# Optimization experiments

Hardware: AMD Instinct MI355X
Metric: run time of the kernel (lower is better)

The kernel has to match this reference:

```python
import jax, jax.numpy as jnp
import numpy as np

N_NODES = 100000
N_EDGES = 6400000


def setup_inputs() -> dict:
    key = jax.random.key(0)
    k1, k2, k3, k4, k5, k6 = jax.random.split(key, 6)
    x = jax.random.normal(k1, (N_NODES, 20), dtype=jnp.float32)
    edge_index = jax.random.randint(k2, (2, N_EDGES), 0, N_NODES, dtype=jnp.int64)
    # Glorot-style init for GCNConv weights, zero bias (PyG default)
    W1 = jax.random.normal(k3, (20, 16), dtype=jnp.float32) * (1.0 / np.sqrt(20))
    b1 = jnp.zeros((16,), dtype=jnp.float32)
    W2 = jax.random.normal(k4, (16, 2), dtype=jnp.float32) * (1.0 / np.sqrt(16))
    b2 = jnp.zeros((2,), dtype=jnp.float32)
    return {"x": x, "edge_index": edge_index, "W1": W1, "b1": b1, "W2": W2, "b2": b2}


def gcn_conv(x, row, col, W, b, num_nodes):
    # x' = D^{-1/2} (A + I) D^{-1/2} X W + b  (PyG GCNConv with self-loops)
    xw = x @ W  # [N, out]
    ones = jnp.ones_like(row, dtype=xw.dtype)
    deg = jax.ops.segment_sum(ones, row, num_segments=num_nodes)  # [N]
    dinv = jnp.where(deg > 0, jax.lax.rsqrt(deg), 0.0)
    norm = dinv[row] * dinv[col]  # [E+N]
    msg = xw[col] * norm[:, None]  # gather + scale
    out = jax.ops.segment_sum(msg, row, num_segments=num_nodes)  # scatter-add
    return out + b


def reference(x, edge_index, W1, b1, W2, b2):
    num_nodes = x.shape[0]
    self_loops = jnp.arange(num_nodes, dtype=edge_index.dtype)
    row = jnp.concatenate([edge_index[0], self_loops])  # target nodes
    col = jnp.concatenate([edge_index[1], self_loops])  # source nodes
    h = gcn_conv(x, row, col, W1, b1, num_nodes)
    h = jax.nn.relu(h)
    # F.dropout(x, training=self.training): identity in eval mode
    h = gcn_conv(h, row, col, W2, b2, num_nodes)
    return jax.nn.log_softmax(h, axis=1)
```

## Files before the change

### kernel.cpp

```cpp
#include <hip/hip_runtime.h>
#include <math.h>


#define XF 20
#define F1 16
#define F2 2
#define RPB 128
#define KMAX 800
#define KP   784
#define TILE 8192
#define EPT 16
#define NJMAX 800
#define CAP 9216
#define BPAD 16

__device__ __forceinline__ unsigned bf16rne(float f) {
    unsigned u = __float_as_uint(f);
    return (u + 0x7FFFu + ((u >> 16) & 1u)) >> 16;
}
__device__ __forceinline__ float bflo(unsigned w) { return __uint_as_float(w << 16); }
__device__ __forceinline__ float bfhi(unsigned w) { return __uint_as_float(w & 0xFFFF0000u); }

__global__ __launch_bounds__(512) void passA_kernel(const int* __restrict__ rows,
                                                    const int* __restrict__ cols,
                                                    int* __restrict__ bhist,
                                                    int* __restrict__ lbt,
                                                    unsigned int* __restrict__ csrtmp,
                                                    int E, int K) {
    __shared__ unsigned int stage[TILE];
    __shared__ int hist[KMAX];
    __shared__ int tsum[512];
    int t = threadIdx.x;
    int bj = blockIdx.x;
    for (int k = t; k < K; k += 512) hist[k] = 0;
    __syncthreads();
    int e0 = bj * TILE;
    int e1 = min(e0 + TILE, E);
    int n = e1 - e0;
    int rloc[EPT];
    #pragma unroll
    for (int it = 0; it < EPT; it++) {
        int e = e0 + it * 512 + t;
        if (e < e1) {
            int r = rows[e];
            rloc[it] = r;
            atomicAdd(&hist[r >> 7], 1);
        }
    }
    __syncthreads();
    int k0 = 2 * t, k1 = 2 * t + 1;
    int v0 = (k0 < K) ? hist[k0] : 0;
    int v1 = (k1 < K) ? hist[k1] : 0;
    int s = v0 + v1;
    tsum[t] = s;
    __syncthreads();
    for (int d = 1; d < 512; d <<= 1) {
        int u = (t >= d) ? tsum[t - d] : 0;
        __syncthreads();
        tsum[t] += u;
        __syncthreads();
    }
    int run = tsum[t] - s;
    long long lrow = (long long)bj * KP;
    if (k0 < K) {
        hist[k0] = run;  lbt[lrow + k0] = run;
        if (v0) atomicAdd(&bhist[k0 * BPAD], v0);
    }
    if (k1 < K) {
        hist[k1] = run + v0;  lbt[lrow + k1] = run + v0;
        if (v1) atomicAdd(&bhist[k1 * BPAD], v1);
    }
    if (t == 0) lbt[lrow + K] = n;
    __syncthreads();
    #pragma unroll
    for (int it = 0; it < EPT; it++) {
        int e = e0 + it * 512 + t;
        if (e < e1) {
            int r = rloc[it];
            int c = cols[e];
            int pos = atomicAdd(&hist[r >> 7], 1);
            stage[pos] = ((unsigned int)c << 7) | (unsigned int)(r & 127);
        }
    }
    __syncthreads();
    for (int ss = t; ss < n; ss += 512)
        csrtmp[(size_t)e0 + ss] = stage[ss];
}

__global__ void bscan_kernel(const int* __restrict__ bhist, int K, int E,
                             int* __restrict__ bbase) {
    __shared__ int tsum[256];
    int t = threadIdx.x;
    int vals[4];
    int s = 0;
    #pragma unroll
    for (int j = 0; j < 4; j++) {
        int idx = t * 4 + j;
        vals[j] = (idx < K) ? bhist[idx * BPAD] : 0;
        s += vals[j];
    }
    tsum[t] = s;
    __syncthreads();
    for (int d = 1; d < 256; d <<= 1) {
        int u = (t >= d) ? tsum[t - d] : 0;
        __syncthreads();
        tsum[t] += u;
        __syncthreads();
    }
    int run = tsum[t] - s;
    #pragma unroll
    for (int j = 0; j < 4; j++) {
        int idx = t * 4 + j;
        if (idx < K) bbase[idx] = run;
        run += vals[j];
    }
    if (t == 0) bbase[K] = E;
}

__global__ __launch_bounds__(512) void passB_kernel(const int* __restrict__ lbt,
                                                    const unsigned int* __restrict__ csrtmp,
                                                    const int* __restrict__ bbase,
                                                    unsigned int* __restrict__ csr,
                                                    int* __restrict__ rowptr,
                                                    float* __restrict__ dinv,
                                                    int N, int K, int E, int nj) {
    __shared__ unsigned int stage[CAP];
    __shared__ int segoff[NJMAX];
    __shared__ int stagepos[NJMAX + 1];
    __shared__ int dcnt[RPB];
    __shared__ int rp[RPB];
    __shared__ int cur[RPB];
    __shared__ int tsum[512];
    int b = blockIdx.x, t = threadIdx.x;
    int lo = b << 7;
    if (t < RPB) { dcnt[t] = 0; cur[t] = 0; }
    int a0 = 2 * t, a1 = 2 * t + 1;
    int la = 0, lb2 = 0;
    if (a0 < nj) {
        const int* lp = lbt + (long long)a0 * KP + b;
        int o0 = lp[0], o1 = lp[1];
        segoff[a0] = o0; la = o1 - o0;
    }
    if (a1 < nj) {
        const int* lp = lbt + (long long)a1 * KP + b;
        int o0 = lp[0], o1 = lp[1];
        segoff[a1] = o0; lb2 = o1 - o0;
    }
    int s = la + lb2;
    tsum[t] = s;
    __syncthreads();
    for (int d = 1; d < 512; d <<= 1) {
        int u = (t >= d) ? tsum[t - d] : 0;
        __syncthreads();
        tsum[t] += u;
        __syncthreads();
    }
    int run = tsum[t] - s;
    if (a0 < nj) stagepos[a0] = run;
    if (a1 < nj) stagepos[a1] = run + la;
    if (t == 511) stagepos[nj] = tsum[511];
    __syncthreads();
    int cnt = min(stagepos[nj], CAP);
    int sw = t >> 3, ln = t & 7;
    for (int seg = sw; seg < nj; seg += 64) {
        int sp = stagepos[seg];
        int len = stagepos[seg + 1] - sp;
        if (sp + len > CAP) len = max(0, CAP - sp);
        size_t src = (size_t)seg * TILE + segoff[seg];
        for (int e2 = ln; e2 < len; e2 += 8) {
            unsigned int p = csrtmp[src + e2];
            stage[sp + e2] = p;
            atomicAdd(&dcnt[p & 127u], 1);
        }
    }
    __syncthreads();
    int gb = bbase[b];
    if (t < 64) {
        int v0 = dcnt[2 * t], v1 = dcnt[2 * t + 1];
        int ss = v0 + v1;
        int sc = ss;
        #pragma unroll
        for (int d = 1; d < 64; d <<= 1) {
            int u = __shfl_up(sc, d);
            if (t >= d) sc += u;
        }
        int excl = gb + sc - ss;
        rp[2 * t] = excl;
        rp[2 * t + 1] = excl + v0;
        int i0 = lo + 2 * t, i1 = i0 + 1;
        if (i0 < N) { rowptr[i0] = excl;      dinv[i0] = rsqrtf((float)v0 + 1.0f); }
        if (i1 < N) { rowptr[i1] = excl + v0; dinv[i1] = rsqrtf((float)v1 + 1.0f); }
        if (t == 0 && b == K - 1) rowptr[N] = E;
    }
    __syncthreads();
    for (int ss = t; ss < cnt; ss += 512) {
        unsigned int p = stage[ss];
        int rr = (int)(p & 127u);
        int dst = rp[rr] + atomicAdd(&cur[rr], 1);
        csr[dst] = p >> 7;
    }
}

__global__ void xw1_kernel(const float* __restrict__ x, const float* __restrict__ W1,
                           const float* __restrict__ dinv, unsigned int* __restrict__ y1h,
                           int N) {
    __shared__ float Ws[XF * F1];
    for (int k = threadIdx.x; k < XF * F1; k += blockDim.x) Ws[k] = W1[k];
    __syncthreads();
    int i = blockIdx.x * blockDim.x + threadIdx.x;
    if (i >= N) return;
    const float4* xv = (const float4*)(x + (size_t)i * XF);
    float xr[XF];
    #pragma unroll
    for (int q = 0; q < 5; q++) {
        float4 v = xv[q];
        xr[q*4+0] = v.x; xr[q*4+1] = v.y; xr[q*4+2] = v.z; xr[q*4+3] = v.w;
    }
    float d = dinv[i];
    float out[F1];
    #pragma unroll
    for (int j = 0; j < F1; j++) {
        float a = 0.f;
        #pragma unroll
        for (int k = 0; k < XF; k++) a += xr[k] * Ws[k * F1 + j];
        out[j] = a * d;
    }
    unsigned int w[8];
    #pragma unroll
    for (int q = 0; q < 8; q++)
        w[q] = bf16rne(out[2*q]) | (bf16rne(out[2*q+1]) << 16);
    uint4* o = (uint4*)(y1h + (size_t)i * 8);
    o[0] = make_uint4(w[0], w[1], w[2], w[3]);
    o[1] = make_uint4(w[4], w[5], w[6], w[7]);
}

__global__ __launch_bounds__(256) void gather16_kernel(const int* __restrict__ rowptr,
                                                       const unsigned int* __restrict__ csr,
                                                       const unsigned int* __restrict__ y1h,
                                                       const float* __restrict__ dinv,
                                                       const float* __restrict__ b1,
                                                       const float* __restrict__ W2,
                                                       float* __restrict__ y2, int N) {
    __shared__ float W2s[F1 * F2];
    if (threadIdx.x < F1 * F2) W2s[threadIdx.x] = W2[threadIdx.x];
    __syncthreads();
    int sub = threadIdx.x >> 5;
    int l = threadIdx.x & 31;
    int i = blockIdx.x * 8 + sub;
    if (i >= N) return;
    int half = l & 1, es = l >> 1;
    int start = rowptr[i], end = rowptr[i + 1];
    const uint4* Y = (const uint4*)y1h;
    float acc[8] = {0.f, 0.f, 0.f, 0.f, 0.f, 0.f, 0.f, 0.f};
    for (int slot = start + es; slot < end; slot += 16) {
        int c = (int)csr[slot];
        uint4 w = Y[(size_t)c * 2 + half];
        acc[0] += bflo(w.x); acc[1] += bfhi(w.x);
        acc[2] += bflo(w.y); acc[3] += bfhi(w.y);
        acc[4] += bflo(w.z); acc[5] += bfhi(w.z);
        acc[6] += bflo(w.w); acc[7] += bfhi(w.w);
    }
    #pragma unroll
    for (int m = 2; m <= 16; m <<= 1) {
        #pragma unroll
        for (int k = 0; k < 8; k++) acc[k] += __shfl_xor(acc[k], m);
    }
    if (l < 2) {
        float d = dinv[i];
        uint4 w = Y[(size_t)i * 2 + l];
        float self[8] = { bflo(w.x), bfhi(w.x), bflo(w.y), bfhi(w.y),
                          bflo(w.z), bfhi(w.z), bflo(w.w), bfhi(w.w) };
        float4 bl = ((const float4*)b1)[l * 2];
        float4 bh = ((const float4*)b1)[l * 2 + 1];
        float bb[8] = { bl.x, bl.y, bl.z, bl.w, bh.x, bh.y, bh.z, bh.w };
        float p0 = 0.f, p1 = 0.f;
        #pragma unroll
        for (int k = 0; k < 8; k++) {
            float hv = fmaxf(d * (acc[k] + self[k]) + bb[k], 0.f);
            p0 += hv * W2s[(l * 8 + k) * 2];
            p1 += hv * W2s[(l * 8 + k) * 2 + 1];
        }
        float q0 = __shfl_xor(p0, 1);
        float q1 = __shfl_xor(p1, 1);
        if (l == 0)
            ((float2*)y2)[i] = make_float2((p0 + q0) * d, (p1 + q1) * d);
    }
}

__global__ __launch_bounds__(256) void gather2_kernel(const int* __restrict__ rowptr,
                                                      const unsigned int* __restrict__ csr,
                                                      const float* __restrict__ y2,
                                                      const float* __restrict__ dinv,
                                                      const float* __restrict__ b2,
                                                      float* __restrict__ out, int N) {
    int sub = threadIdx.x >> 5;
    int l = threadIdx.x & 31;
    int i = blockIdx.x * 8 + sub;
    if (i >= N) return;
    int start = rowptr[i], end = rowptr[i + 1];
    float a0 = 0.f, a1 = 0.f;
    for (int slot = start + l; slot < end; slot += 32) {
        int c = (int)csr[slot];
        float2 v = ((const float2*)y2)[c];
        a0 += v.x;
        a1 += v.y;
    }
    #pragma unroll
    for (int m = 16; m > 0; m >>= 1) {
        a0 += __shfl_xor(a0, m);
        a1 += __shfl_xor(a1, m);
    }
    if (l == 0) {
        float d = dinv[i];
        float2 yi = ((const float2*)y2)[i];
        float v0 = d * (a0 + yi.x) + b2[0];
        float v1 = d * (a1 + yi.y) + b2[1];
        float mm = fmaxf(v0, v1);
        float lse = mm + logf(expf(v0 - mm) + expf(v1 - mm));
        ((float2*)out)[i] = make_float2(v0 - lse, v1 - lse);
    }
}

static inline size_t align256(size_t x) { return (x + 255) & ~(size_t)255; }

extern "C" void kernel_launch(void* const* d_in, const int* in_sizes, int n_in,
                              void* d_out, int out_size, void* d_ws, size_t ws_size,
                              hipStream_t stream) {
    const float* x  = (const float*)d_in[0];
    const int*   ei = (const int*)d_in[1];
    const float* W1 = (const float*)d_in[2];
    const float* b1 = (const float*)d_in[3];
    const float* W2 = (const float*)d_in[4];
    const float* b2 = (const float*)d_in[5];
    float* out = (float*)d_out;

    const int N = in_sizes[0] / XF;
    const int E = in_sizes[1] / 2;
    const int* rows = ei;
    const int* cols = ei + E;
    const int K = (N + RPB - 1) >> 7;
    const int nj = (E + TILE - 1) / TILE;

    char* ws = (char*)d_ws;
    size_t off = 0;
    int*   bhist   = (int*)(ws + off);   off = align256(off + (size_t)KMAX * BPAD * 4);
    size_t zero_bytes = off;
    int*   bbase   = (int*)(ws + off);   off = align256(off + (size_t)(KMAX + 1) * 4);
    int*   rowptr  = (int*)(ws + off);   off = align256(off + (size_t)(N + 1) * 4);
    float* dinv    = (float*)(ws + off); off = align256(off + (size_t)N * 4);
    int*   lbt     = (int*)(ws + off);   off = align256(off + (size_t)nj * KP * 4);
    unsigned int* csr = (unsigned int*)(ws + off); off = align256(off + (size_t)E * 4);
    size_t tmp0 = off;
    unsigned int* csrtmp = (unsigned int*)(ws + tmp0);
    unsigned int* y1h = (unsigned int*)(ws + tmp0);
    float* y2 = (float*)(ws + align256(tmp0 + (size_t)N * 8 * 4));

    hipMemsetAsync(d_ws, 0, zero_bytes, stream);

    const int B = 256;
    const int nbN = (N + B - 1) / B;
    const int nbW = (N + 7) / 8;

    passA_kernel<<<nj, 512, 0, stream>>>(rows, cols, bhist, lbt, csrtmp, E, K);
    bscan_kernel<<<1, B, 0, stream>>>(bhist, K, E, bbase);
    passB_kernel<<<K, 512, 0, stream>>>(lbt, csrtmp, bbase, csr, rowptr, dinv, N, K, E, nj);
    xw1_kernel<<<nbN, B, 0, stream>>>(x, W1, dinv, y1h, N);
    gather16_kernel<<<nbW, B, 0, stream>>>(rowptr, csr, y1h, dinv, b1, W2, y2, N);
    gather2_kernel<<<nbW, B, 0, stream>>>(rowptr, csr, y2, dinv, b2, out, N);
}
```

Before: 278.0 us.

## Transpose bucket offset table and privatize passB histogram across four sub-groups

Adds a tiled transpose kernel so passB can read each block's per-tile segment offsets contiguously with int2 loads, replacing strided column reads. passB now copies edges into shared memory first, then counts them in four padded per-thread-group histograms to cut LDS atomic contention. The scatter uses per-group cursors derived from the combined prefix sums. In exchange it adds an extra kernel launch, extra workspace, and an extra pass over the shared-memory stage.

New measurement: 283.9 us. +2.1%, slower.

```diff
diff --git a/kernel.cpp b/kernel.cpp
--- a/kernel.cpp
+++ b/kernel.cpp
@@ -8,6 +8,7 @@
 #define RPB 128
 #define KMAX 800
 #define KP   784
+#define NJP  800
 #define TILE 8192
 #define EPT 16
 #define NJMAX 800
@@ -117,7 +118,31 @@
     if (t == 0) bbase[K] = E;
 }
 
-__global__ __launch_bounds__(512) void passB_kernel(const int* __restrict__ lbt,
+__global__ __launch_bounds__(256) void transpose_kernel(const int* __restrict__ lbt,
+                                                        int* __restrict__ lbtT,
+                                                        int nj, int K) {
+    __shared__ int tile[64][65];
+    int tx = threadIdx.x & 63, ty = threadIdx.x >> 6;
+    int bk = blockIdx.x * 64;
+    int bb = blockIdx.y * 64;
+    #pragma unroll
+    for (int r = 0; r < 16; r++) {
+        int row = bb + ty * 16 + r;
+        int col = bk + tx;
+        if (row < nj && col <= K)
+            tile[ty * 16 + r][tx] = lbt[(long long)row * KP + col];
+    }
+    __syncthreads();
+    #pragma unroll
+    for (int r = 0; r < 16; r++) {
+        int orow = bk + ty * 16 + r;
+        int ocol = bb + tx;
+        if (orow <= K && ocol < nj)
+            lbtT[(long long)orow * NJP + ocol] = tile[tx][ty * 16 + r];
+    }
+}
+
+__global__ __launch_bounds__(512) void passB_kernel(const int* __restrict__ lbtT,
                                                     const unsigned int* __restrict__ csrtmp,
                                                     const int* __restrict__ bbase,
                                                     unsigned int* __restrict__ csr,
@@ -127,24 +152,24 @@
     __shared__ unsigned int stage[CAP];
     __shared__ int segoff[NJMAX];
     __shared__ int stagepos[NJMAX + 1];
-    __shared__ int dcnt[RPB];
-    __shared__ int rp[RPB];
-    __shared__ int cur[RPB];
+    __shared__ int dcnt4[4 * 132];
+    __shared__ int cur4[4 * 132];
+    __shared__ int rp4[4 * 128];
     __shared__ int tsum[512];
     int b = blockIdx.x, t = threadIdx.x;
     int lo = b << 7;
-    if (t < RPB) { dcnt[t] = 0; cur[t] = 0; }
-    int a0 = 2 * t, a1 = 2 * t + 1;
+    for (int k = t; k < 4 * 132; k += 512) { dcnt4[k] = 0; cur4[k] = 0; }
+    int a0 = 2 * t, a1 = a0 + 1;
     int la = 0, lb2 = 0;
-    if (a0 < nj) {
-        const int* lp = lbt + (long long)a0 * KP + b;
-        int o0 = lp[0], o1 = lp[1];
-        segoff[a0] = o0; la = o1 - o0;
-    }
     if (a1 < nj) {
-        const int* lp = lbt + (long long)a1 * KP + b;
-        int o0 = lp[0], o1 = lp[1];
-        segoff[a1] = o0; lb2 = o1 - o0;
+        int2 s2 = ((const int2*)(lbtT + (long long)b * NJP))[t];
+        int2 e2 = ((const int2*)(lbtT + (long long)(b + 1) * NJP))[t];
+        segoff[a0] = s2.x; segoff[a1] = s2.y;
+        la = e2.x - s2.x;  lb2 = e2.y - s2.y;
+    } else if (a0 < nj) {
+        int o0 = lbtT[(long long)b * NJP + a0];
+        segoff[a0] = o0;
+        la = lbtT[(long long)(b + 1) * NJP + a0] - o0;
     }
     int s = la + lb2;
     tsum[t] = s;
@@ -167,36 +192,44 @@
         int len = stagepos[seg + 1] - sp;
         if (sp + len > CAP) len = max(0, CAP - sp);
         size_t src = (size_t)seg * TILE + segoff[seg];
-        for (int e2 = ln; e2 < len; e2 += 8) {
-            unsigned int p = csrtmp[src + e2];
-            stage[sp + e2] = p;
-            atomicAdd(&dcnt[p & 127u], 1);
-        }
-    }
+        for (int e2 = ln; e2 < len; e2 += 8)
+            stage[sp + e2] = csrtmp[src + e2];
+    }
+    __syncthreads();
+    int g = t >> 7;
+    for (int ss = t; ss < cnt; ss += 512)
+        atomicAdd(&dcnt4[g * 132 + (int)(stage[ss] & 127u)], 1);
     __syncthreads();
     int gb = bbase[b];
     if (t < 64) {
-        int v0 = dcnt[2 * t], v1 = dcnt[2 * t + 1];
-        int ss = v0 + v1;
-        int sc = ss;
+        int r0 = 2 * t, r1 = r0 + 1;
+        int c00 = dcnt4[r0], c10 = dcnt4[132 + r0], c20 = dcnt4[264 + r0], c30 = dcnt4[396 + r0];
+        int c01 = dcnt4[r1], c11 = dcnt4[132 + r1], c21 = dcnt4[264 + r1], c31 = dcnt4[396 + r1];
+        int v0 = c00 + c10 + c20 + c30;
+        int v1 = c01 + c11 + c21 + c31;
+        int ssum = v0 + v1;
+        int sc = ssum;
         #pragma unroll
         for (int d = 1; d < 64; d <<= 1) {
             int u = __shfl_up(sc, d);
             if (t >= d) sc += u;
         }
-        int excl = gb + sc - ss;
-        rp[2 * t] = excl;
-        rp[2 * t + 1] = excl + v0;
-        int i0 = lo + 2 * t, i1 = i0 + 1;
-        if (i0 < N) { rowptr[i0] = excl;      dinv[i0] = rsqrtf((float)v0 + 1.0f); }
-        if (i1 < N) { rowptr[i1] = excl + v0; dinv[i1] = rsqrtf((float)v1 + 1.0f); }
+        int excl = gb + sc - ssum;
+        rp4[r0] = excl;            rp4[128 + r0] = excl + c00;
+        rp4[256 + r0] = excl + c00 + c10;  rp4[384 + r0] = excl + c00 + c10 + c20;
+        int e1b = excl + v0;
+        rp4[r1] = e1b;             rp4[128 + r1] = e1b + c01;
+        rp4[256 + r1] = e1b + c01 + c11;   rp4[384 + r1] = e1b + c01 + c11 + c21;
+        int i0 = lo + r0, i1 = lo + r1;
+        if (i0 < N) { rowptr[i0] = excl; dinv[i0] = rsqrtf((float)v0 + 1.0f); }
+        if (i1 < N) { rowptr[i1] = e1b;  dinv[i1] = rsqrtf((float)v1 + 1.0f); }
         if (t == 0 && b == K - 1) rowptr[N] = E;
     }
     __syncthreads();
     for (int ss = t; ss < cnt; ss += 512) {
         unsigned int p = stage[ss];
         int rr = (int)(p & 127u);
-        int dst = rp[rr] + atomicAdd(&cur[rr], 1);
+        int dst = rp4[g * 128 + rr] + atomicAdd(&cur4[g * 132 + rr], 1);
         csr[dst] = p >> 7;
     }
 }
@@ -349,6 +382,7 @@
     int*   rowptr  = (int*)(ws + off);   off = align256(off + (size_t)(N + 1) * 4);
     float* dinv    = (float*)(ws + off); off = align256(off + (size_t)N * 4);
     int*   lbt     = (int*)(ws + off);   off = align256(off + (size_t)nj * KP * 4);
+    int*   lbtT    = (int*)(ws + off);   off = align256(off + (size_t)(KMAX + 1) * NJP * 4);
     unsigned int* csr = (unsigned int*)(ws + off); off = align256(off + (size_t)E * 4);
     size_t tmp0 = off;
     unsigned int* csrtmp = (unsigned int*)(ws + tmp0);
@@ -363,7 +397,11 @@
 
     passA_kernel<<<nj, 512, 0, stream>>>(rows, cols, bhist, lbt, csrtmp, E, K);
     bscan_kernel<<<1, B, 0, stream>>>(bhist, K, E, bbase);
-    passB_kernel<<<K, 512, 0, stream>>>(lbt, csrtmp, bbase, csr, rowptr, dinv, N, K, E, nj);
+    {
+        dim3 tg((K + 1 + 63) / 64, (nj + 63) / 64);
+        transpose_kernel<<<tg, B, 0, stream>>>(lbt, lbtT, nj, K);
+    }
+    passB_kernel<<<K, 512, 0, stream>>>(lbtT, csrtmp, bbase, csr, rowptr, dinv, N, K, E, nj);
     xw1_kernel<<<nbN, B, 0, stream>>>(x, W1, dinv, y1h, N);
     gather16_kernel<<<nbW, B, 0, stream>>>(rowptr, csr, y1h, dinv, b1, W2, y2, N);
     gather2_kernel<<<nbW, B, 0, stream>>>(rowptr, csr, y2, dinv, b2, out, N);
```
